# Performance work log

Hardware: AMD Instinct MI355X
Metric: run time of the kernel (lower is better)

## Reference

```python
import jax, jax.numpy as jnp
import numpy as np
from jax.scipy.linalg import expm

EPS = 1e-5  # torch LayerNorm default

def _layernorm(x, g, b):
    m = x.mean(-1, keepdims=True)
    v = ((x - m) ** 2).mean(-1, keepdims=True)
    return (x - m) / jnp.sqrt(v + EPS) * g + b

def setup_inputs() -> dict:
    H, S, K = 1024, 64, 3
    B, T = 4, 4096
    key = jax.random.key(0)
    ks = jax.random.split(key, 12)
    sc = 0.02
    inp = {
        'x': jax.random.normal(ks[0], (B, T, H), jnp.float32),
        'A': -jnp.abs(jax.random.normal(ks[1], (S, S), jnp.float32) * sc),
        'dt_A': jnp.asarray(0.1, jnp.float32),
        'B_w': jax.random.normal(ks[2], (S, H), jnp.float32) * sc,
        'B_b': jnp.zeros((S,), jnp.float32),
        'C_w': jax.random.normal(ks[3], (S, H), jnp.float32) * sc,
        'C_b': jnp.zeros((S,), jnp.float32),
        'D_w': jax.random.normal(ks[4], (H, S), jnp.float32) * sc,
        'D_b': jnp.zeros((H,), jnp.float32),
        'conv_w': jax.random.normal(ks[5], (H, 1, K), jnp.float32) * sc,  # depthwise
        'conv_b': jnp.zeros((H,), jnp.float32),
        'gate_w': jax.random.normal(ks[6], (2 * H, H), jnp.float32) * sc,
        'gate_b': jnp.zeros((2 * H,), jnp.float32),
        'ln_in_g': jnp.ones((H,), jnp.float32),
        'ln_in_b': jnp.zeros((H,), jnp.float32),
        'ln_st_g': jnp.ones((S,), jnp.float32),
        'ln_st_b': jnp.zeros((S,), jnp.float32),
    }
    return inp

def reference(x, A, dt_A, B_w, B_b, C_w, C_b, D_w, D_b, conv_w, conv_b,
              gate_w, gate_b, ln_in_g, ln_in_b, ln_st_g, ln_st_b):
    Bt, T, H = x.shape
    K = conv_w.shape[-1]
    pad = K // 2
    x_norm = _layernorm(x, ln_in_g, ln_in_b)  # [B,T,H]
    # depthwise conv1d (groups = H), 'same' padding, residual add
    xc = jnp.transpose(x_norm, (0, 2, 1))  # [B,H,T]
    xc = jax.lax.conv_general_dilated(
        xc, conv_w, window_strides=(1,), padding=[(pad, pad)],
        dimension_numbers=('NCH', 'OIH', 'NCH'), feature_group_count=H)
    xc = xc + conv_b[None, :, None]
    x_norm = x_norm + jnp.transpose(xc, (0, 2, 1))
    # gating
    gate_all = x_norm @ gate_w.T + gate_b  # [B,T,2H]
    gate, input_gate = gate_all[..., :H], gate_all[..., H:]
    gate = jax.nn.sigmoid(gate)
    # input-dependent B, C
    Bm = (x_norm * jax.nn.sigmoid(input_gate)) @ B_w.T + B_b  # [B,T,S]
    Cm = x_norm @ C_w.T + C_b                                  # [B,T,S]
    A_bar = expm(dt_A * A)  # [S,S]
    # sequential recurrence over time via scan
    def step(state, bc):
        b_t, c_t = bc
        s = state @ A_bar + b_t
        s = _layernorm(s, ln_st_g, ln_st_b)
        return s, c_t * s
    state0 = jnp.zeros((Bt, A.shape[0]), x.dtype)
    _, ys = jax.lax.scan(step, state0,
                         (jnp.transpose(Bm, (1, 0, 2)), jnp.transpose(Cm, (1, 0, 2))))
    ssm = jnp.transpose(ys, (1, 0, 2))  # [B,T,S]
    ssm = ssm @ D_w.T + D_b             # [B,T,H]
    return ssm * gate
```

## Files before the change

### kernel.cpp

```cpp
#include <hip/hip_runtime.h>
#include <cstdint>

#define EPS 1e-5f
typedef float f32x4 __attribute__((ext_vector_type(4)));
typedef short bf8 __attribute__((ext_vector_type(8)));
typedef unsigned short u16;
typedef unsigned short u16x8 __attribute__((ext_vector_type(8)));
typedef unsigned int uint4v __attribute__((ext_vector_type(4)));

__device__ __forceinline__ u16 f2b(float f){
  unsigned x = __float_as_uint(f);
  unsigned r = x + 0x7FFFu + ((x>>16)&1u);
  return (u16)(r>>16);
}
__device__ __forceinline__ float b2f(u16 h){ return __uint_as_float(((unsigned)h)<<16); }
__device__ __forceinline__ unsigned pk2(float a, float b){
  unsigned ua = __float_as_uint(a) + 0x8000u;
  unsigned ub = __float_as_uint(b) + 0x8000u;
  return __builtin_amdgcn_perm(ub, ua, 0x07060302u);
}

#define GLL(gp, lp) __builtin_amdgcn_global_load_lds((__attribute__((address_space(1))) const void*)(gp), (__attribute__((address_space(3))) void*)(lp), 16, 0, 0)

__global__ __launch_bounds__(1024) void k_prep(const float* __restrict__ A, const float* __restrict__ dtp,
    const float* __restrict__ stg, const float* __restrict__ stb,
    float* __restrict__ abeta, u16* __restrict__ ft)
{
  __shared__ float M[4096], Ta[4096], Tb[4096], P[4096];
  __shared__ float cmn[64];
  int tid = threadIdx.x;
  float dt = dtp[0];
  for (int e=tid; e<4096; e+=1024){
    float v = dt * A[e];
    int i = e>>6, j = e&63;
    M[e] = v;
    P[e] = v + (i==j ? 1.0f : 0.0f);
    Ta[e] = v;
  }
  __syncthreads();
  float* src = Ta; float* dst = Tb;
  for (int k=2;k<=14;k++){
    float inv = 1.0f/(float)k;
    int i = tid>>4, j0 = (tid&15)*4;
    float a0=0,a1=0,a2=0,a3=0;
    for (int m2=0;m2<64;m2++){
      float f = src[i*64+m2];
      const float* Mr = &M[m2*64+j0];
      a0 += f*Mr[0]; a1 += f*Mr[1]; a2 += f*Mr[2]; a3 += f*Mr[3];
    }
    a0*=inv; a1*=inv; a2*=inv; a3*=inv;
    int base=i*64+j0;
    dst[base+0]=a0; dst[base+1]=a1; dst[base+2]=a2; dst[base+3]=a3;
    P[base+0]+=a0; P[base+1]+=a1; P[base+2]+=a2; P[base+3]+=a3;
    __syncthreads();
    float* tmp=src; src=dst; dst=tmp;
  }
  if (tid<64){
    float c0=0, ab=0; int p = tid;
    for (int q2=0;q2<64;q2++){ float ap = P[q2*64+p]; c0 += stg[q2]*ap; ab += stb[q2]*ap; }
    cmn[p] = c0*(1.0f/64.0f);
    abeta[p] = ab;
  }
  __syncthreads();
  for (int e=tid; e<4096; e+=1024){
    int q2=e>>6, p=e&63;
    Ta[e] = stg[q2]*P[q2*64+p] - cmn[p];
  }
  __syncthreads();
  for (int ii=0; ii<4; ii++){
    int e = tid*4+ii;
    int j = e&7, l = (e>>3)&63, kt=(e>>9)&1, mt=e>>10;
    int q2 = 16*(2*kt + (j>>2)) + 4*(l>>4) + (j&3);
    int p = 16*mt + (l&15);
    float v = Ta[q2*64+p];
    u16 hi = f2b(v);
    float lo = v - b2f(hi);
    ft[e] = hi;
    ft[e+4096] = f2b(lo);
  }
}

__global__ __launch_bounds__(256) void k_wcvt(const float* __restrict__ gw, const float* __restrict__ bw,
   const float* __restrict__ cw, const float* __restrict__ dw,
   u16* __restrict__ ogw, u16* __restrict__ obw, u16* __restrict__ ocw, u16* __restrict__ odw)
{
  int n = (blockIdx.x*256 + threadIdx.x)*4;
  const float* src; u16* dst; int off;
  if (n < 2097152){ src=gw; dst=ogw; off=n; }
  else if (n < 2162688){ src=bw; dst=obw; off=n-2097152; }
  else if (n < 2228224){ src=cw; dst=ocw; off=n-2162688; }
  else { src=dw; dst=odw; off=n-2228224; }
  f32x4 v = *(const f32x4*)(src+off);
  uint2 pkv;
  pkv.x = (unsigned)f2b(v.x) | ((unsigned)f2b(v.y)<<16);
  pkv.y = (unsigned)f2b(v.z) | ((unsigned)f2b(v.w)<<16);
  *(uint2*)(dst+off) = pkv;
}

__global__ __launch_bounds__(256) void k_lnconv(const float* __restrict__ x, const float* __restrict__ gin,
  const float* __restrict__ bin, const float* __restrict__ cwt, const float* __restrict__ cb, u16* __restrict__ xn)
{
  __shared__ float red[10][8];
  int tid = threadIdx.x; int w = tid>>6; int lane = tid&63;
  int r0 = blockIdx.x*8;
  int bt = r0>>12, t0 = r0&4095;
  int c4 = tid*4;
  f32x4 g4 = *(const f32x4*)(gin + c4);
  f32x4 b4 = *(const f32x4*)(bin + c4);
  f32x4 vals[10];
  for (int lr=0; lr<10; lr++){
    int t = t0 - 1 + lr;
    f32x4 xv = {0,0,0,0};
    bool ok = (t>=0 && t<4096);
    if (ok) xv = *(const f32x4*)(x + (size_t)(bt*4096+t)*1024 + c4);
    float s = xv.x+xv.y+xv.z+xv.w;
    float q = xv.x*xv.x+xv.y*xv.y+xv.z*xv.z+xv.w*xv.w;
    for (int m2=1;m2<=32;m2<<=1){ s += __shfl_xor(s,m2,64); q += __shfl_xor(q,m2,64); }
    if (lane==0){ red[lr][w]=s; red[lr][4+w]=q; }
    __syncthreads();
    s = red[lr][0]+red[lr][1]+red[lr][2]+red[lr][3];
    q = red[lr][4]+red[lr][5]+red[lr][6]+red[lr][7];
    float mu = s*(1.f/1024.f);
    float var = q*(1.f/1024.f) - mu*mu;
    float rr = rsqrtf(var + EPS);
    f32x4 o = {0,0,0,0};
    if (ok){
      o.x=(xv.x-mu)*rr*g4.x+b4.x; o.y=(xv.y-mu)*rr*g4.y+b4.y;
      o.z=(xv.z-mu)*rr*g4.z+b4.z; o.w=(xv.w-mu)*rr*g4.w+b4.w;
    }
    vals[lr]=o;
  }
  float w0[4], w1[4], w2[4], cbv[4];
  for (int ii=0;ii<4;ii++){ int c = c4+ii; w0[ii]=cwt[c*3+0]; w1[ii]=cwt[c*3+1]; w2[ii]=cwt[c*3+2]; cbv[ii]=cb[c]; }
  for (int lr=1; lr<=8; lr++){
    int t = t0 + lr - 1;
    f32x4 o;
    o.x = vals[lr].x + w0[0]*vals[lr-1].x + w1[0]*vals[lr].x + w2[0]*vals[lr+1].x + cbv[0];
    o.y = vals[lr].y + w0[1]*vals[lr-1].y + w1[1]*vals[lr].y + w2[1]*vals[lr+1].y + cbv[1];
    o.z = vals[lr].z + w0[2]*vals[lr-1].z + w1[2]*vals[lr].z + w2[2]*vals[lr+1].z + cbv[2];
    o.w = vals[lr].w + w0[3]*vals[lr-1].w + w1[3]*vals[lr].w + w2[3]*vals[lr+1].w + cbv[3];
    size_t off = (size_t)(bt*4096+t)*1024 + c4;
    unsigned lo2 = (unsigned)f2b(o.x) | ((unsigned)f2b(o.y)<<16);
    unsigned hi2 = (unsigned)f2b(o.z) | ((unsigned)f2b(o.w)<<16);
    uint2 pk; pk.x=lo2; pk.y=hi2;
    *(uint2*)(xn + off) = pk;
  }
}

__global__ __launch_bounds__(256) void k_gate(const u16* __restrict__ xn, const u16* __restrict__ gw,
    const float* __restrict__ gb, u16* __restrict__ gate_o, u16* __restrict__ xg_o)
{
  __shared__ char smem[33792];
  u16* As = (u16*)smem;
  u16* Bs = (u16*)(smem + 8192);
  float* st = (float*)smem;
  int tid=threadIdx.x, w=tid>>6, l=tid&63;
  int flat = blockIdx.x + (int)gridDim.x*blockIdx.y;
  int logical = (flat&7)*256 + (flat>>3);
  int n0 = (logical&15)*128, m0 = (logical>>4)*128;
  int wr = w>>1, wc = w&1;
  f32x4 acc[4][4] = {};
  for (int kk=0; kk<32; kk++){
    int k0 = kk*32;
    for (int i2=0;i2<2;i2++){
      const char* ga = (const char*)xn + ((size_t)(m0+32*w+16*i2+(l>>2))*1024 + k0)*2 + (l&3)*16;
      GLL(ga, (char*)As + (32*w+16*i2)*64);
      const char* gbp = (const char*)gw + ((size_t)(n0+32*w+16*i2+(l>>2))*1024 + k0)*2 + (l&3)*16;
      GLL(gbp, (char*)Bs + (32*w+16*i2)*64);
    }
    __syncthreads();
    bf8 af[4], bfr[4];
    for (int mt=0;mt<4;mt++) af[mt] = *(const bf8*)(As + (wr*64+mt*16+(l&15))*32 + 8*(l>>4));
    for (int nt=0;nt<4;nt++) bfr[nt] = *(const bf8*)(Bs + (wc*64+nt*16+(l&15))*32 + 8*(l>>4));
    for (int mt=0;mt<4;mt++) for (int nt=0;nt<4;nt++)
      acc[mt][nt] = __builtin_amdgcn_mfma_f32_16x16x32_bf16(af[mt], bfr[nt], acc[mt][nt], 0,0,0);
    __syncthreads();
  }
  bool isxg = (n0 >= 1024);
  int r2 = tid>>2, q = tid&3;
  f32x4 gb4[8];
  for (int j=0;j<8;j++) gb4[j] = *(const f32x4*)(gb + n0 + q*32 + j*4);
  int g = l>>4, c = l&15;
  for (int p=0;p<2;p++){
    __syncthreads();
    if (wr==p){
      for (int mt=0;mt<4;mt++) for (int nt=0;nt<4;nt++)
        for (int r=0;r<4;r++)
          st[(mt*16+4*g+r)*132 + wc*64+nt*16+c] = acc[mt][nt][r];
    }
    __syncthreads();
    int row = m0 + p*64 + r2;
    const float* sp = st + r2*132 + q*32;
    u16 ob[32];
    if (!isxg){
      for (int j=0;j<8;j++){
        f32x4 v = *(const f32x4*)(sp + 4*j);
        v = v + gb4[j];
        ob[4*j+0] = f2b(1.0f/(1.0f+__expf(-v.x)));
        ob[4*j+1] = f2b(1.0f/(1.0f+__expf(-v.y)));
        ob[4*j+2] = f2b(1.0f/(1.0f+__expf(-v.z)));
        ob[4*j+3] = f2b(1.0f/(1.0f+__expf(-v.w)));
      }
    } else {
      const u16* xp = xn + (size_t)row*1024 + (n0-1024) + q*32;
      u16 xb[32];
      for (int j=0;j<4;j++){
        u16x8 t8 = *(const u16x8*)(xp + 8*j);
        for (int e=0;e<8;e++) xb[8*j+e] = t8[e];
      }
      for (int j=0;j<8;j++){
        f32x4 v = *(const f32x4*)(sp + 4*j);
        v = v + gb4[j];
        ob[4*j+0] = f2b(b2f(xb[4*j+0]) * (1.0f/(1.0f+__expf(-v.x))));
        ob[4*j+1] = f2b(b2f(xb[4*j+1]) * (1.0f/(1.0f+__expf(-v.y))));
        ob[4*j+2] = f2b(b2f(xb[4*j+2]) * (1.0f/(1.0f+__expf(-v.z))));
        ob[4*j+3] = f2b(b2f(xb[4*j+3]) * (1.0f/(1.0f+__expf(-v.w))));
      }
    }
    u16* op = isxg ? (xg_o + (size_t)row*1024 + (n0-1024) + q*32)
                   : (gate_o + (size_t)row*1024 + n0 + q*32);
    unsigned od[16];
    for (int i2=0;i2<16;i2++) od[i2] = (unsigned)ob[2*i2] | ((unsigned)ob[2*i2+1]<<16);
    uint4v s0 = {od[0],od[1],od[2],od[3]};
    uint4v s1 = {od[4],od[5],od[6],od[7]};
    uint4v s2 = {od[8],od[9],od[10],od[11]};
    uint4v s3 = {od[12],od[13],od[14],od[15]};
    *(uint4v*)(op+ 0) = s0;
    *(uint4v*)(op+ 8) = s1;
    *(uint4v*)(op+16) = s2;
    *(uint4v*)(op+24) = s3;
  }
}

__global__ __launch_bounds__(256) void k_bc(const u16* __restrict__ xg, const u16* __restrict__ xn,
   const u16* __restrict__ bw, const u16* __restrict__ cw,
   const float* __restrict__ bb, const float* __restrict__ cbias_, const float* __restrict__ abeta,
   float* __restrict__ c_ws, u16* __restrict__ cm)
{
  __shared__ u16 As[128*32], Bs[64*32];
  int tid=threadIdx.x, w=tid>>6, l=tid&63;
  int id = blockIdx.x; int half = id>>7; int m0 = (id&127)*128;
  const u16* Ap = half ? xn : xg;
  const u16* Bp = half ? cw : bw;
  f32x4 acc[2][4]={};
  for (int kk=0;kk<32;kk++){
    int k0=kk*32;
    for (int i2=0;i2<2;i2++){
      const char* ga=(const char*)Ap + ((size_t)(m0+32*w+16*i2+(l>>2))*1024+k0)*2+(l&3)*16;
      GLL(ga, (char*)As+(32*w+16*i2)*64);
    }
    { const char* gbp=(const char*)Bp + ((size_t)(16*w+(l>>2))*1024+k0)*2+(l&3)*16;
      GLL(gbp, (char*)Bs+(16*w)*64); }
    __syncthreads();
    bf8 af[2], bfr[4];
    for (int mt=0;mt<2;mt++) af[mt]=*(const bf8*)(As+(32*w+16*mt+(l&15))*32+8*(l>>4));
    for (int nt=0;nt<4;nt++) bfr[nt]=*(const bf8*)(Bs+(16*nt+(l&15))*32+8*(l>>4));
    for (int mt=0;mt<2;mt++) for(int nt=0;nt<4;nt++)
      acc[mt][nt]=__builtin_amdgcn_mfma_f32_16x16x32_bf16(af[mt],bfr[nt],acc[mt][nt],0,0,0);
    __syncthreads();
  }
  int g=l>>4, c=l&15;
  if (half==0){
    for (int nt=0;nt<4;nt++){ int n=16*nt+c; float bias=bb[n]; float ab=abeta[n];
      for(int mt=0;mt<2;mt++) for(int r=0;r<4;r++){
        int row=m0+32*w+16*mt+4*g+r; int bt=row>>12, t=row&4095;
        float v=acc[mt][nt][r]+bias + (t>0?ab:0.0f);
        c_ws[(size_t)t*256 + bt*64 + n] = v;
      }
    }
  } else {
    for (int nt=0;nt<4;nt++){ int n=16*nt+c; float bias=cbias_[n];
      for(int mt=0;mt<2;mt++) for(int r=0;r<4;r++){
        int row=m0+32*w+16*mt+4*g+r;
        cm[(size_t)row*64+n]=f2b(acc[mt][nt][r]+bias);
      }
    }
  }
}

__global__ __launch_bounds__(64,1) void k_scan(const float* __restrict__ c_ws, const u16* __restrict__ ft,
  float* __restrict__ z_ws)
{
  __shared__ float ring[16*256];
  int l=threadIdx.x, g=l>>4, b=l&3;
  const bf8* ftv=(const bf8*)ft;
  bf8 Wh[4][2], Wl[4][2];
  for(int mt=0;mt<4;mt++)for(int kt=0;kt<2;kt++){
    Wh[mt][kt]=ftv[(mt*2+kt)*64+l];
    Wl[mt][kt]=ftv[(8+mt*2+kt)*64+l];
  }
  const f32x4 zed = {0.f,0.f,0.f,0.f};
  f32x4 z0,z1,z2,z3;
  {
    const float* zp = c_ws + b*64 + 4*g;
    z0=*(const f32x4*)(zp+0); z1=*(const f32x4*)(zp+16); z2=*(const f32x4*)(zp+32); z3=*(const f32x4*)(zp+48);
  }
  for(int u2=1;u2<=8;u2++){
    const char* ga=(const char*)c_ws + (size_t)u2*1024 + l*16;
    GLL(ga, (char*)ring + u2*1024);
  }
  asm volatile("s_waitcnt vmcnt(0)" ::: "memory");
  unsigned laneoff;
  {
    __attribute__((address_space(3))) float* l3=( __attribute__((address_space(3))) float*)ring;
    laneoff=(unsigned)(uintptr_t)l3 + (unsigned)(b*256 + g*16);
  }
  unsigned voff = (unsigned)(((l&15)*64 + 4*g)*4);
  unsigned long long zb = (unsigned long long)(uintptr_t)z_ws;
  f32x4 cN0,cN1,cN2,cN3;
  bf8 zf0, zf1;

  {
    uint4v p0,p1;
    p0.x=pk2(z0.x,z0.y); p0.y=pk2(z0.z,z0.w); p0.z=pk2(z1.x,z1.y); p0.w=pk2(z1.z,z1.w);
    p1.x=pk2(z2.x,z2.y); p1.y=pk2(z2.z,z2.w); p1.z=pk2(z3.x,z3.y); p1.w=pk2(z3.z,z3.w);
    { union { uint4v u; bf8 h; } cv; cv.u=p0; zf0=cv.h; cv.u=p1; zf1=cv.h; }
  }

  unsigned slotr = 1024u;
  unsigned ldst  = 9u*1024u;
  const char* gsrc = (const char*)c_ws + (size_t)9*1024;

  for (int t=0; t<4096; ++t){
    asm volatile("s_waitcnt vmcnt(24)" ::: "memory");
    { unsigned ro = laneoff + slotr;
      asm volatile("ds_read_b128 %0, %4 offset:0\n\t"
                   "ds_read_b128 %1, %4 offset:64\n\t"
                   "ds_read_b128 %2, %4 offset:128\n\t"
                   "ds_read_b128 %3, %4 offset:192"
                   : "=v"(cN0),"=v"(cN1),"=v"(cN2),"=v"(cN3) : "v"(ro) : "memory"); }
    GLL(gsrc + (size_t)l*16, (char*)ring + ldst);
    f32x4 u0=__builtin_amdgcn_mfma_f32_16x16x32_bf16(Wh[0][0],zf0,zed,0,0,0);
    f32x4 u1=__builtin_amdgcn_mfma_f32_16x16x32_bf16(Wh[1][0],zf0,zed,0,0,0);
    f32x4 u2=__builtin_amdgcn_mfma_f32_16x16x32_bf16(Wh[2][0],zf0,zed,0,0,0);
    f32x4 u3=__builtin_amdgcn_mfma_f32_16x16x32_bf16(Wh[3][0],zf0,zed,0,0,0);
    u0=__builtin_amdgcn_mfma_f32_16x16x32_bf16(Wh[0][1],zf1,u0,0,0,0);
    u1=__builtin_amdgcn_mfma_f32_16x16x32_bf16(Wh[1][1],zf1,u1,0,0,0);
    u2=__builtin_amdgcn_mfma_f32_16x16x32_bf16(Wh[2][1],zf1,u2,0,0,0);
    u3=__builtin_amdgcn_mfma_f32_16x16x32_bf16(Wh[3][1],zf1,u3,0,0,0);
    u0=__builtin_amdgcn_mfma_f32_16x16x32_bf16(Wl[0][0],zf0,u0,0,0,0);
    u1=__builtin_amdgcn_mfma_f32_16x16x32_bf16(Wl[1][0],zf0,u1,0,0,0);
    u2=__builtin_amdgcn_mfma_f32_16x16x32_bf16(Wl[2][0],zf0,u2,0,0,0);
    u3=__builtin_amdgcn_mfma_f32_16x16x32_bf16(Wl[3][0],zf0,u3,0,0,0);
    u0=__builtin_amdgcn_mfma_f32_16x16x32_bf16(Wl[0][1],zf1,u0,0,0,0);
    u1=__builtin_amdgcn_mfma_f32_16x16x32_bf16(Wl[1][1],zf1,u1,0,0,0);
    u2=__builtin_amdgcn_mfma_f32_16x16x32_bf16(Wl[2][1],zf1,u2,0,0,0);
    u3=__builtin_amdgcn_mfma_f32_16x16x32_bf16(Wl[3][1],zf1,u3,0,0,0);
    float rr;
    {
      f32x4 s4=(z0+z1)+(z2+z3);
      float s=(s4.x+s4.y)+(s4.z+s4.w);
      f32x4 qa=z0*z0; qa=z1*z1+qa;
      f32x4 qb=z2*z2; qb=z3*z3+qb;
      f32x4 q4=qa+qb;
      float q=(q4.x+q4.y)+(q4.z+q4.w);
      float sB=s, qB=q;
      asm("v_permlane16_swap_b32 %0, %1" : "+v"(s), "+v"(sB));
      asm("v_permlane16_swap_b32 %0, %1" : "+v"(q), "+v"(qB));
      s+=sB; q+=qB;
      float sC=s, qC=q;
      asm("v_permlane32_swap_b32 %0, %1" : "+v"(s), "+v"(sC));
      asm("v_permlane32_swap_b32 %0, %1" : "+v"(q), "+v"(qC));
      s+=sC; q+=qC;
      float mu=s*(1.f/64.f);
      float var=q*(1.f/64.f)-mu*mu;
      rr=rsqrtf(var+EPS);
    }
    asm volatile("global_store_dwordx4 %0, %1, %5\n\t"
                 "global_store_dwordx4 %0, %2, %5 offset:64\n\t"
                 "global_store_dwordx4 %0, %3, %5 offset:128\n\t"
                 "global_store_dwordx4 %0, %4, %5 offset:192"
                 :: "v"(voff), "v"(z0), "v"(z1), "v"(z2), "v"(z3), "s"(zb) : "memory");
    voff += 4096u;
    slotr = (slotr + 1024u) & 16383u;
    ldst  = (ldst  + 1024u) & 16383u;
    gsrc += 1024;
    asm volatile("s_waitcnt lgkmcnt(0)" : "+v"(cN0),"+v"(cN1),"+v"(cN2),"+v"(cN3) :: "memory");
    z0 = u0*rr + cN0;
    z1 = u1*rr + cN1;
    z2 = u2*rr + cN2;
    z3 = u3*rr + cN3;
    uint4v p0,p1;
    p0.x=pk2(z0.x,z0.y); p0.y=pk2(z0.z,z0.w); p0.z=pk2(z1.x,z1.y); p0.w=pk2(z1.z,z1.w);
    p1.x=pk2(z2.x,z2.y); p1.y=pk2(z2.z,z2.w); p1.z=pk2(z3.x,z3.y); p1.w=pk2(z3.z,z3.w);
    { union { uint4v u; bf8 h; } cv; cv.u=p0; zf0=cv.h; cv.u=p1; zf1=cv.h; }
  }
}

__global__ __launch_bounds__(256) void k_y(const float* __restrict__ z_ws, const u16* __restrict__ cm,
  const float* __restrict__ stg, const float* __restrict__ stb, u16* __restrict__ y)
{
  int tid=threadIdx.x, w=tid>>6, l=tid&63;
  int token = blockIdx.x*4 + w;
  int bt = token>>12, t = token&4095;
  float zv = z_ws[(size_t)t*1024 + bt*64 + l];
  float s=zv, q=zv*zv;
  for (int m2=1;m2<=32;m2<<=1){ s += __shfl_xor(s,m2,64); q += __shfl_xor(q,m2,64); }
  float mu=s*(1.f/64.f), var=q*(1.f/64.f)-mu*mu, rr=rsqrtf(var+EPS);
  float sv=(zv-mu)*rr*stg[l]+stb[l];
  y[(size_t)token*64 + l] = f2b(sv * b2f(cm[(size_t)token*64+l]));
}

__global__ __launch_bounds__(256) void k_out(const u16* __restrict__ y, const u16* __restrict__ dw,
   const float* __restrict__ db, const u16* __restrict__ gate, float* __restrict__ out)
{
  __shared__ float tr[4][16][68];
  int tid=threadIdx.x, w=tid>>6, l=tid&63, g=l>>4, c=l&15;
  int n0=blockIdx.x*64, m0=blockIdx.y*64;
  int mrow = m0 + 16*w + c;
  bf8 af0=*(const bf8*)(y + (size_t)mrow*64 + 8*g);
  bf8 af1=*(const bf8*)(y + (size_t)mrow*64 + 32 + 8*g);
  f32x4 acc[4];
  for(int nt=0;nt<4;nt++){
    int n=n0+16*nt+c;
    bf8 b0=*(const bf8*)(dw + (size_t)n*64 + 8*g);
    bf8 b1=*(const bf8*)(dw + (size_t)n*64 + 32 + 8*g);
    f32x4 a={0,0,0,0};
    a=__builtin_amdgcn_mfma_f32_16x16x32_bf16(af0,b0,a,0,0,0);
    a=__builtin_amdgcn_mfma_f32_16x16x32_bf16(af1,b1,a,0,0,0);
    acc[nt]=a+db[n];
  }
  for(int nt=0;nt<4;nt++) for(int r=0;r<4;r++) tr[w][4*g+r][16*nt+c]=acc[nt][r];
  __syncthreads();
  int lr=l>>2, cc0=(l&3)*16;
  int grow=m0+16*w+lr;
  const u16* gp = gate + (size_t)grow*1024 + n0 + cc0;
  u16x8 g0=*(const u16x8*)(gp), g1=*(const u16x8*)(gp+8);
  float* op = out + (size_t)grow*1024 + n0 + cc0;
  float vv[16];
  for(int j2=0;j2<16;j2++){
    u16 gb16 = (j2<8)? g0[j2] : g1[j2-8];
    vv[j2]=tr[w][lr][cc0+j2]*b2f(gb16);
  }
  for(int j2=0;j2<4;j2++){
    f32x4 ov={vv[4*j2],vv[4*j2+1],vv[4*j2+2],vv[4*j2+3]};
    *(f32x4*)(op+4*j2)=ov;
  }
}

extern "C" void kernel_launch(void* const* d_in, const int* in_sizes, int n_in,
                              void* d_out, int out_size, void* d_ws, size_t ws_size,
                              hipStream_t stream) {
  const float* x=(const float*)d_in[0];
  const float* A=(const float*)d_in[1];
  const float* dt=(const float*)d_in[2];
  const float* B_w=(const float*)d_in[3];
  const float* B_b=(const float*)d_in[4];
  const float* C_w=(const float*)d_in[5];
  const float* C_b=(const float*)d_in[6];
  const float* D_w=(const float*)d_in[7];
  const float* D_b=(const float*)d_in[8];
  const float* conv_w=(const float*)d_in[9];
  const float* conv_b=(const float*)d_in[10];
  const float* gate_w=(const float*)d_in[11];
  const float* gate_b=(const float*)d_in[12];
  const float* ln_in_g=(const float*)d_in[13];
  const float* ln_in_b=(const float*)d_in[14];
  const float* ln_st_g=(const float*)d_in[15];
  const float* ln_st_b=(const float*)d_in[16];
  char* ws=(char*)d_ws;
  u16* xn   =(u16*)(ws);
  u16* xg   =(u16*)(ws+33554432);
  u16* gate =(u16*)(ws+67108864);
  u16* gwb  =(u16*)(ws+100663296);
  u16* bwb  =(u16*)(ws+104857600);
  u16* cwb  =(u16*)(ws+104988672);
  u16* dwb  =(u16*)(ws+105119744);
  u16* cm   =(u16*)(ws+105250816);
  float* c_ws=(float*)(ws+107347968);
  float* z_ws=(float*)(ws+111558656);
  u16* y    =(u16*)(ws+128335872);
  float* abeta=(float*)(ws+130433024);
  u16* ft   =(u16*)(ws+130433280);
  float* out=(float*)d_out;

  hipLaunchKernelGGL(k_prep,  dim3(1),      dim3(1024),0,stream, A, dt, ln_st_g, ln_st_b, abeta, ft);
  hipLaunchKernelGGL(k_wcvt,  dim3(2240),   dim3(256), 0,stream, gate_w,B_w,C_w,D_w, gwb,bwb,cwb,dwb);
  hipLaunchKernelGGL(k_lnconv,dim3(2048),   dim3(256), 0,stream, x, ln_in_g, ln_in_b, conv_w, conv_b, xn);
  hipLaunchKernelGGL(k_gate,  dim3(16,128), dim3(256), 0,stream, xn,gwb,gate_b,gate,xg);
  hipLaunchKernelGGL(k_bc,    dim3(256),    dim3(256), 0,stream, xg,xn,bwb,cwb,B_b,C_b,abeta,c_ws,cm);
  hipLaunchKernelGGL(k_scan,  dim3(1),      dim3(64),  0,stream, c_ws, ft, z_ws);
  hipLaunchKernelGGL(k_y,     dim3(4096),   dim3(256), 0,stream, z_ws,cm,ln_st_g,ln_st_b,y);
  hipLaunchKernelGGL(k_out,   dim3(16,256), dim3(256), 0,stream, y,dwb,D_b,gate,out);
}
```

Measured before the change: 1.715 ms.

## Overlap sequential scan with gate and C GEMMs in one fused launch

The single-block sequential scan is moved into a combined launch whose other blocks compute the sigmoid gate half of the gating GEMM and the C projection. Neither of those depends on the scan. Only the input-gate half and the B projection, which the scan needs, run beforehand. The weight conversion is also merged into the matrix-exponential prep kernel to save a launch. The aim is to hide the latency-bound one-block scan behind independent GEMM work. The risk is that the scan block shares its compute unit and memory bandwidth with GEMM blocks and may be scheduled late or run slower.

```diff
diff --git a/kernel.cpp b/kernel.cpp
--- a/kernel.cpp
+++ b/kernel.cpp
@@ -22,10 +22,27 @@
 
 #define GLL(gp, lp) __builtin_amdgcn_global_load_lds((__attribute__((address_space(1))) const void*)(gp), (__attribute__((address_space(3))) void*)(lp), 16, 0, 0)
 
-__global__ __launch_bounds__(1024) void k_prep(const float* __restrict__ A, const float* __restrict__ dtp,
+__global__ __launch_bounds__(1024) void k_prepw(const float* __restrict__ A, const float* __restrict__ dtp,
     const float* __restrict__ stg, const float* __restrict__ stb,
-    float* __restrict__ abeta, u16* __restrict__ ft)
-{
+    float* __restrict__ abeta, u16* __restrict__ ft,
+    const float* __restrict__ gw, const float* __restrict__ bw,
+    const float* __restrict__ cw, const float* __restrict__ dw,
+    u16* __restrict__ ogw, u16* __restrict__ obw, u16* __restrict__ ocw, u16* __restrict__ odw)
+{
+  if (blockIdx.x != 0){
+    int n = ((int)(blockIdx.x-1)*1024 + (int)threadIdx.x)*4;
+    const float* src; u16* dst; int off;
+    if (n < 2097152){ src=gw; dst=ogw; off=n; }
+    else if (n < 2162688){ src=bw; dst=obw; off=n-2097152; }
+    else if (n < 2228224){ src=cw; dst=ocw; off=n-2162688; }
+    else { src=dw; dst=odw; off=n-2228224; }
+    f32x4 v = *(const f32x4*)(src+off);
+    uint2 pkv;
+    pkv.x = (unsigned)f2b(v.x) | ((unsigned)f2b(v.y)<<16);
+    pkv.y = (unsigned)f2b(v.z) | ((unsigned)f2b(v.w)<<16);
+    *(uint2*)(dst+off) = pkv;
+    return;
+  }
   __shared__ float M[4096], Ta[4096], Tb[4096], P[4096];
   __shared__ float cmn[64];
   int tid = threadIdx.x;
@@ -78,23 +95,6 @@
     ft[e] = hi;
     ft[e+4096] = f2b(lo);
   }
-}
-
-__global__ __launch_bounds__(256) void k_wcvt(const float* __restrict__ gw, const float* __restrict__ bw,
-   const float* __restrict__ cw, const float* __restrict__ dw,
-   u16* __restrict__ ogw, u16* __restrict__ obw, u16* __restrict__ ocw, u16* __restrict__ odw)
-{
-  int n = (blockIdx.x*256 + threadIdx.x)*4;
-  const float* src; u16* dst; int off;
-  if (n < 2097152){ src=gw; dst=ogw; off=n; }
-  else if (n < 2162688){ src=bw; dst=obw; off=n-2097152; }
-  else if (n < 2228224){ src=cw; dst=ocw; off=n-2162688; }
-  else { src=dw; dst=odw; off=n-2228224; }
-  f32x4 v = *(const f32x4*)(src+off);
-  uint2 pkv;
-  pkv.x = (unsigned)f2b(v.x) | ((unsigned)f2b(v.y)<<16);
-  pkv.y = (unsigned)f2b(v.z) | ((unsigned)f2b(v.w)<<16);
-  *(uint2*)(dst+off) = pkv;
 }
 
 __global__ __launch_bounds__(256) void k_lnconv(const float* __restrict__ x, const float* __restrict__ gin,
@@ -147,17 +147,14 @@
   }
 }
 
-__global__ __launch_bounds__(256) void k_gate(const u16* __restrict__ xn, const u16* __restrict__ gw,
-    const float* __restrict__ gb, u16* __restrict__ gate_o, u16* __restrict__ xg_o)
-{
-  __shared__ char smem[33792];
+__device__ __forceinline__ void gate_body(char* smem, int tid, int n0, int m0, bool isxg,
+    const u16* __restrict__ xn, const u16* __restrict__ gw, const float* __restrict__ gb,
+    u16* __restrict__ outp)
+{
   u16* As = (u16*)smem;
   u16* Bs = (u16*)(smem + 8192);
   float* st = (float*)smem;
-  int tid=threadIdx.x, w=tid>>6, l=tid&63;
-  int flat = blockIdx.x + (int)gridDim.x*blockIdx.y;
-  int logical = (flat&7)*256 + (flat>>3);
-  int n0 = (logical&15)*128, m0 = (logical>>4)*128;
+  int w=tid>>6, l=tid&63;
   int wr = w>>1, wc = w&1;
   f32x4 acc[4][4] = {};
   for (int kk=0; kk<32; kk++){
@@ -176,7 +173,6 @@
       acc[mt][nt] = __builtin_amdgcn_mfma_f32_16x16x32_bf16(af[mt], bfr[nt], acc[mt][nt], 0,0,0);
     __syncthreads();
   }
-  bool isxg = (n0 >= 1024);
   int r2 = tid>>2, q = tid&3;
   f32x4 gb4[8];
   for (int j=0;j<8;j++) gb4[j] = *(const f32x4*)(gb + n0 + q*32 + j*4);
@@ -217,8 +213,8 @@
         ob[4*j+3] = f2b(b2f(xb[4*j+3]) * (1.0f/(1.0f+__expf(-v.w))));
       }
     }
-    u16* op = isxg ? (xg_o + (size_t)row*1024 + (n0-1024) + q*32)
-                   : (gate_o + (size_t)row*1024 + n0 + q*32);
+    int ncol = isxg ? (n0-1024) : n0;
+    u16* op = outp + (size_t)row*1024 + ncol + q*32;
     unsigned od[16];
     for (int i2=0;i2<16;i2++) od[i2] = (unsigned)ob[2*i2] | ((unsigned)ob[2*i2+1]<<16);
     uint4v s0 = {od[0],od[1],od[2],od[3]};
@@ -232,24 +228,21 @@
   }
 }
 
-__global__ __launch_bounds__(256) void k_bc(const u16* __restrict__ xg, const u16* __restrict__ xn,
-   const u16* __restrict__ bw, const u16* __restrict__ cw,
-   const float* __restrict__ bb, const float* __restrict__ cbias_, const float* __restrict__ abeta,
-   float* __restrict__ c_ws, u16* __restrict__ cm)
-{
-  __shared__ u16 As[128*32], Bs[64*32];
-  int tid=threadIdx.x, w=tid>>6, l=tid&63;
-  int id = blockIdx.x; int half = id>>7; int m0 = (id&127)*128;
-  const u16* Ap = half ? xn : xg;
-  const u16* Bp = half ? cw : bw;
+__device__ __forceinline__ void cm_body(char* smem, int tid, int m0,
+  const u16* __restrict__ xn, const u16* __restrict__ cw, const float* __restrict__ cbias_,
+  u16* __restrict__ cm)
+{
+  u16* As = (u16*)smem;
+  u16* Bs = (u16*)(smem + 8192);
+  int w=tid>>6, l=tid&63;
   f32x4 acc[2][4]={};
   for (int kk=0;kk<32;kk++){
     int k0=kk*32;
     for (int i2=0;i2<2;i2++){
-      const char* ga=(const char*)Ap + ((size_t)(m0+32*w+16*i2+(l>>2))*1024+k0)*2+(l&3)*16;
+      const char* ga=(const char*)xn + ((size_t)(m0+32*w+16*i2+(l>>2))*1024+k0)*2+(l&3)*16;
       GLL(ga, (char*)As+(32*w+16*i2)*64);
     }
-    { const char* gbp=(const char*)Bp + ((size_t)(16*w+(l>>2))*1024+k0)*2+(l&3)*16;
+    { const char* gbp=(const char*)cw + ((size_t)(16*w+(l>>2))*1024+k0)*2+(l&3)*16;
       GLL(gbp, (char*)Bs+(16*w)*64); }
     __syncthreads();
     bf8 af[2], bfr[4];
@@ -260,29 +253,79 @@
     __syncthreads();
   }
   int g=l>>4, c=l&15;
-  if (half==0){
-    for (int nt=0;nt<4;nt++){ int n=16*nt+c; float bias=bb[n]; float ab=abeta[n];
-      for(int mt=0;mt<2;mt++) for(int r=0;r<4;r++){
-        int row=m0+32*w+16*mt+4*g+r; int bt=row>>12, t=row&4095;
-        float v=acc[mt][nt][r]+bias + (t>0?ab:0.0f);
-        c_ws[(size_t)t*256 + bt*64 + n] = v;
-      }
-    }
-  } else {
-    for (int nt=0;nt<4;nt++){ int n=16*nt+c; float bias=cbias_[n];
-      for(int mt=0;mt<2;mt++) for(int r=0;r<4;r++){
-        int row=m0+32*w+16*mt+4*g+r;
-        cm[(size_t)row*64+n]=f2b(acc[mt][nt][r]+bias);
-      }
-    }
-  }
-}
-
-__global__ __launch_bounds__(64,1) void k_scan(const float* __restrict__ c_ws, const u16* __restrict__ ft,
-  float* __restrict__ z_ws)
-{
-  __shared__ float ring[16*256];
-  int l=threadIdx.x, g=l>>4, b=l&3;
+  for (int nt=0;nt<4;nt++){ int n=16*nt+c; float bias=cbias_[n];
+    for(int mt=0;mt<2;mt++) for(int r=0;r<4;r++){
+      int row=m0+32*w+16*mt+4*g+r;
+      cm[(size_t)row*64+n]=f2b(acc[mt][nt][r]+bias);
+    }
+  }
+}
+
+__global__ __launch_bounds__(256) void k_gate_xg(const u16* __restrict__ xn, const u16* __restrict__ gw,
+    const float* __restrict__ gb, u16* __restrict__ xg_o)
+{
+  __shared__ char smem[33792];
+  int flat = blockIdx.x;
+  int logical = (flat&7)*128 + (flat>>3);
+  int n0 = 1024 + (logical&7)*128, m0 = (logical>>3)*128;
+  gate_body(smem, threadIdx.x, n0, m0, true, xn, gw, gb, xg_o);
+}
+
+__global__ __launch_bounds__(256) void k_bc_bm(const u16* __restrict__ xg, const u16* __restrict__ bw,
+   const float* __restrict__ bb, const float* __restrict__ abeta, float* __restrict__ c_ws)
+{
+  __shared__ u16 As[128*32], Bs[64*32];
+  int tid=threadIdx.x, w=tid>>6, l=tid&63;
+  int m0 = blockIdx.x*128;
+  f32x4 acc[2][4]={};
+  for (int kk=0;kk<32;kk++){
+    int k0=kk*32;
+    for (int i2=0;i2<2;i2++){
+      const char* ga=(const char*)xg + ((size_t)(m0+32*w+16*i2+(l>>2))*1024+k0)*2+(l&3)*16;
+      GLL(ga, (char*)As+(32*w+16*i2)*64);
+    }
+    { const char* gbp=(const char*)bw + ((size_t)(16*w+(l>>2))*1024+k0)*2+(l&3)*16;
+      GLL(gbp, (char*)Bs+(16*w)*64); }
+    __syncthreads();
+    bf8 af[2], bfr[4];
+    for (int mt=0;mt<2;mt++) af[mt]=*(const bf8*)(As+(32*w+16*mt+(l&15))*32+8*(l>>4));
+    for (int nt=0;nt<4;nt++) bfr[nt]=*(const bf8*)(Bs+(16*nt+(l&15))*32+8*(l>>4));
+    for (int mt=0;mt<2;mt++) for(int nt=0;nt<4;nt++)
+      acc[mt][nt]=__builtin_amdgcn_mfma_f32_16x16x32_bf16(af[mt],bfr[nt],acc[mt][nt],0,0,0);
+    __syncthreads();
+  }
+  int g=l>>4, c=l&15;
+  for (int nt=0;nt<4;nt++){ int n=16*nt+c; float bias=bb[n]; float ab=abeta[n];
+    for(int mt=0;mt<2;mt++) for(int r=0;r<4;r++){
+      int row=m0+32*w+16*mt+4*g+r; int bt=row>>12, t=row&4095;
+      float v=acc[mt][nt][r]+bias + (t>0?ab:0.0f);
+      c_ws[(size_t)t*256 + bt*64 + n] = v;
+    }
+  }
+}
+
+__global__ __launch_bounds__(256) void k_fused(const float* __restrict__ c_ws, const u16* __restrict__ ft,
+  float* __restrict__ z_ws,
+  const u16* __restrict__ xn, const u16* __restrict__ gw, const float* __restrict__ gb,
+  u16* __restrict__ gate_o,
+  const u16* __restrict__ cw, const float* __restrict__ cbias_, u16* __restrict__ cm)
+{
+  __shared__ char smem[33792];
+  int bid = blockIdx.x, tid = threadIdx.x;
+  if (bid > 1024){
+    cm_body(smem, tid, (bid-1025)*128, xn, cw, cbias_, cm);
+    return;
+  }
+  if (bid >= 1){
+    int flat = bid-1;
+    int logical = (flat&7)*128 + (flat>>3);
+    int n0 = (logical&7)*128, m0 = (logical>>3)*128;
+    gate_body(smem, tid, n0, m0, false, xn, gw, gb, gate_o);
+    return;
+  }
+  if (tid >= 64) return;
+  float* ring = (float*)smem;
+  int l=tid, g=l>>4, b=l&3;
   const bf8* ftv=(const bf8*)ft;
   bf8 Wh[4][2], Wl[4][2];
   for(int mt=0;mt<4;mt++)for(int kt=0;kt<2;kt++){
@@ -474,12 +517,13 @@
   u16* ft   =(u16*)(ws+130433280);
   float* out=(float*)d_out;
 
-  hipLaunchKernelGGL(k_prep,  dim3(1),      dim3(1024),0,stream, A, dt, ln_st_g, ln_st_b, abeta, ft);
-  hipLaunchKernelGGL(k_wcvt,  dim3(2240),   dim3(256), 0,stream, gate_w,B_w,C_w,D_w, gwb,bwb,cwb,dwb);
+  hipLaunchKernelGGL(k_prepw, dim3(561),    dim3(1024),0,stream, A, dt, ln_st_g, ln_st_b, abeta, ft,
+                                                            gate_w,B_w,C_w,D_w, gwb,bwb,cwb,dwb);
   hipLaunchKernelGGL(k_lnconv,dim3(2048),   dim3(256), 0,stream, x, ln_in_g, ln_in_b, conv_w, conv_b, xn);
-  hipLaunchKernelGGL(k_gate,  dim3(16,128), dim3(256), 0,stream, xn,gwb,gate_b,gate,xg);
-  hipLaunchKernelGGL(k_bc,    dim3(256),    dim3(256), 0,stream, xg,xn,bwb,cwb,B_b,C_b,abeta,c_ws,cm);
-  hipLaunchKernelGGL(k_scan,  dim3(1),      dim3(64),  0,stream, c_ws, ft, z_ws);
+  hipLaunchKernelGGL(k_gate_xg,dim3(1024),  dim3(256), 0,stream, xn,gwb,gate_b,xg);
+  hipLaunchKernelGGL(k_bc_bm, dim3(128),    dim3(256), 0,stream, xg,bwb,B_b,abeta,c_ws);
+  hipLaunchKernelGGL(k_fused, dim3(1153),   dim3(256), 0,stream, c_ws, ft, z_ws,
+                                                            xn,gwb,gate_b,gate, cwb,C_b,cm);
   hipLaunchKernelGGL(k_y,     dim3(4096),   dim3(256), 0,stream, z_ws,cm,ln_st_g,ln_st_b,y);
   hipLaunchKernelGGL(k_out,   dim3(16,256), dim3(256), 0,stream, y,dwb,D_b,gate,out);
 }
```

Measured after the change: 1.664 ms. 2.9% less time.
